# Performance work log

Hardware: AMD Instinct MI355X
Metric: run time of the kernel (lower is better)

The kernel has to match this reference:

```python
import jax, jax.numpy as jnp
import numpy as np
import math

MODEL_DIM = 1024
HEAD_DIM = 64
NUM_HEADS = 16
FF_MULT = 4
FF_DIM = FF_MULT * MODEL_DIM
ATTN_DIM = NUM_HEADS * HEAD_DIM
FUSED_DIMS = (ATTN_DIM, ATTN_DIM, ATTN_DIM, FF_DIM, FF_DIM)


def setup_inputs() -> dict:
    key = jax.random.key(0)
    k_x, k_in, k_attn, k_ff = jax.random.split(key, 4)
    B, S = 2, 2048
    inputs = jax.random.normal(k_x, (B, S, MODEL_DIM), dtype=jnp.float32)
    # LayerNorm affine params (torch defaults: weight=1, bias=0)
    ln_w = jnp.ones((MODEL_DIM,), dtype=jnp.float32)
    ln_b = jnp.zeros((MODEL_DIM,), dtype=jnp.float32)
    # Linear weights stored as [in, out] (equivalent to torch W.T)
    s_in = 1.0 / math.sqrt(MODEL_DIM)
    w_in = jax.random.uniform(k_in, (MODEL_DIM, sum(FUSED_DIMS)), jnp.float32, -s_in, s_in)
    s_a = 1.0 / math.sqrt(ATTN_DIM)
    w_attn = jax.random.uniform(k_attn, (ATTN_DIM, MODEL_DIM), jnp.float32, -s_a, s_a)
    s_f = 1.0 / math.sqrt(FF_DIM)
    w_ff = jax.random.uniform(k_ff, (FF_DIM, MODEL_DIM), jnp.float32, -s_f, s_f)
    return {"inputs": inputs, "ln_w": ln_w, "ln_b": ln_b,
            "w_in": w_in, "w_attn": w_attn, "w_ff": w_ff}


def _layer_norm(x, w, b, eps=1e-5):
    mu = jnp.mean(x, axis=-1, keepdims=True)
    var = jnp.var(x, axis=-1, keepdims=True)
    return (x - mu) * jax.lax.rsqrt(var + eps) * w + b


def reference(inputs, ln_w, ln_b, w_in, w_attn, w_ff):
    B, S, D = inputs.shape
    units = _layer_norm(inputs, ln_w, ln_b)
    proj = units @ w_in                                   # [B,S,3*A+2*F]
    splits = np.cumsum(FUSED_DIMS)[:-1]
    q, k, v, ff, ff_gate = jnp.split(proj, splits, axis=-1)
    # split heads: [B,S,H*d] -> [B,H,S,d]
    def heads(t):
        return t.reshape(B, S, NUM_HEADS, HEAD_DIM).transpose(0, 2, 1, 3)
    q, k, v = heads(q), heads(k), heads(v)
    scale = 1.0 / math.sqrt(HEAD_DIM)
    score = jnp.einsum('bhsd,bhTd->bhsT', q, k) * scale   # [B,H,S,S]
    weight = jax.nn.softmax(score, axis=-1)
    attn = jnp.einsum('bhsT,bhTd->bhsd', weight, v)       # [B,H,S,d]
    concat = attn.transpose(0, 2, 1, 3).reshape(B, S, ATTN_DIM)
    attn_out = concat @ w_attn                            # [B,S,D]
    ff_out = (ff * jax.nn.gelu(ff_gate, approximate=True)) @ w_ff
    return inputs + attn_out + ff_out
```

## Files before the change

### kernel.cpp

```cpp
#include <hip/hip_runtime.h>
#include <hip/hip_bf16.h>
#include <cstdint>
#include <cstddef>

typedef __bf16 bf16;
typedef __bf16 bf16x8 __attribute__((ext_vector_type(8)));
typedef float f32x4 __attribute__((ext_vector_type(4)));

#define MFMA16(a, b, c) __builtin_amdgcn_mfma_f32_16x16x32_bf16(a, b, c, 0, 0, 0)

#define GLOBAL_LOAD_LDS16(gptr, lptr)                                          \
  __builtin_amdgcn_global_load_lds(                                            \
      (const __attribute__((address_space(1))) void*)(gptr),                   \
      (__attribute__((address_space(3))) void*)(lptr), 16, 0, 0)

__global__ __launch_bounds__(256) void prep(const float* __restrict__ w_in,
                                            const float* __restrict__ w_attn,
                                            const float* __restrict__ w_ff,
                                            bf16* __restrict__ wt_in,
                                            bf16* __restrict__ wtcat,
                                            const float* __restrict__ x,
                                            const float* __restrict__ ln_w,
                                            const float* __restrict__ ln_b,
                                            bf16* __restrict__ xn) {
  __shared__ __align__(16) float t[64][65];
  const int tid = threadIdx.x;
  if (blockIdx.x < 4096) {
    int id = blockIdx.x;
    const float* src; bf16* dst;
    int srcN, n0, k0, kcol0;
    size_t LDO;
    bool win;
    if (id < 2816) {
      src = w_in; dst = wt_in; srcN = 11264; LDO = 1024;
      n0 = (id % 176) * 64; k0 = (id / 176) * 64; kcol0 = 0; win = true;
    } else if (id < 3072) {
      id -= 2816; src = w_attn; dst = wtcat; srcN = 1024; LDO = 5120;
      n0 = (id % 16) * 64; k0 = (id / 16) * 64; kcol0 = 0; win = false;
    } else {
      id -= 3072; src = w_ff; dst = wtcat; srcN = 1024; LDO = 5120;
      n0 = (id % 16) * 64; k0 = (id / 16) * 64; kcol0 = 1024; win = false;
    }
    int drow0;
    if (!win || n0 < 3072) {
      drow0 = n0;
    } else if (n0 < 7168) {
      int m = n0 - 3072; drow0 = 3072 + ((m >> 6) << 7);
    } else {
      int m = n0 - 7168; drow0 = 3072 + ((m >> 6) << 7) + 64;
    }
#pragma unroll
    for (int i = 0; i < 16; i++) {
      int k = i * 4 + (tid >> 6), n = tid & 63;
      t[k][n] = src[(size_t)(k0 + k) * srcN + n0 + n];
    }
    __syncthreads();
#pragma unroll
    for (int j = 0; j < 2; j++) {
      int n = j * 32 + (tid >> 3), kc = (tid & 7) * 8;
      bf16x8 o;
#pragma unroll
      for (int u = 0; u < 8; u++) o[u] = (bf16)t[kc + u][n];
      *(bf16x8*)&dst[(size_t)(drow0 + n) * LDO + kcol0 + k0 + kc] = o;
    }
  } else {
    __shared__ float rs[256], rss[256];
    const int row = blockIdx.x - 4096;
    const float* xr = x + (size_t)row * 1024;
    float4 v = *(const float4*)&xr[tid * 4];
    float s = v.x + v.y + v.z + v.w;
    float ss = v.x * v.x + v.y * v.y + v.z * v.z + v.w * v.w;
    rs[tid] = s; rss[tid] = ss;
    __syncthreads();
    for (int off = 128; off > 0; off >>= 1) {
      if (tid < off) { rs[tid] += rs[tid + off]; rss[tid] += rss[tid + off]; }
      __syncthreads();
    }
    const float mean = rs[0] * (1.f / 1024.f);
    const float var = rss[0] * (1.f / 1024.f) - mean * mean;
    const float rstd = rsqrtf(var + 1e-5f);
    const float* vp = (const float*)&v;
    for (int i = 0; i < 4; i++) {
      int c = tid * 4 + i;
      xn[(size_t)row * 1024 + c] = (bf16)((vp[i] - mean) * rstd * ln_w[c] + ln_b[c]);
    }
  }
}

__global__ __launch_bounds__(512, 4) void flash_attn(const bf16* __restrict__ proj,
                                                     const bf16* __restrict__ vt,
                                                     bf16* __restrict__ hcat) {
  __shared__ __align__(16) char smem[67584];
  bf16* Ks = (bf16*)smem;
  bf16* Vs = (bf16*)(smem + 16384);
  bf16* Ps = (bf16*)(smem + 32768);
  const int tid = threadIdx.x;
  const int wave = tid >> 6, lane = tid & 63;
  const int quad = lane >> 4, l16 = lane & 15;
  const int q0 = blockIdx.x * 128;
  const int h = blockIdx.y, b = blockIdx.z;
  constexpr size_t LDP = 3072;
  const bf16* Qb = proj + (size_t)b * 2048 * LDP + h * 64;
  const bf16* Kb = proj + (size_t)b * 2048 * LDP + 1024 + h * 64;
  const bf16* Vt = vt + (size_t)(b * 16 + h) * 64 * 2048;

  const int qrow = q0 + wave * 16 + l16;
  bf16x8 aq0r = *(const bf16x8*)&Qb[(size_t)qrow * LDP + quad * 8];
  bf16x8 aq1r = *(const bf16x8*)&Qb[(size_t)qrow * LDP + 32 + quad * 8];
  bf16x8 aq0, aq1;
#pragma unroll
  for (int i = 0; i < 8; i++) {
    aq0[i] = (bf16)((float)aq0r[i] * 0.125f);
    aq1[i] = (bf16)((float)aq1r[i] * 0.125f);
  }

  f32x4 O[4] = {};
  float plrow[4] = {0.f, 0.f, 0.f, 0.f};

  const int krow_ = wave * 8 + (lane >> 3);
  const int kq_ = ((lane & 7) ^ (krow_ & 7)) * 8;
  const int vrow_ = wave * 4 + (lane >> 4);
  const int vq_ = ((lane & 15) ^ (vrow_ & 15)) * 8;

  for (int j0 = 0; j0 < 2048; j0 += 128) {
#pragma unroll
    for (int p = 0; p < 2; p++) {
      int kr = p * 64 + krow_;
      GLOBAL_LOAD_LDS16(&Kb[(size_t)(j0 + kr) * LDP + kq_],
                        &Ks[kr * 64 + (lane & 7) * 8]);
      int vr = p * 32 + vrow_;
      GLOBAL_LOAD_LDS16(&Vt[(size_t)vr * 2048 + j0 + vq_],
                        &Vs[vr * 128 + (lane & 15) * 8]);
    }
    __syncthreads();

    f32x4 sa[8];
#pragma unroll
    for (int nt = 0; nt < 8; nt++) {
      int r = nt * 16 + l16;
      bf16x8 bk0 = *(const bf16x8*)&Ks[r * 64 + (quad ^ (r & 7)) * 8];
      bf16x8 bk1 = *(const bf16x8*)&Ks[r * 64 + ((quad + 4) ^ (r & 7)) * 8];
      f32x4 t = {};
      t = MFMA16(aq0, bk0, t);
      sa[nt] = MFMA16(aq1, bk1, t);
    }

    bf16* Pw = Ps + wave * (16 * 136);
#pragma unroll
    for (int r = 0; r < 4; r++) {
      bf16* pr = &Pw[(quad * 4 + r) * 136];
      float ts = 0.f;
#pragma unroll
      for (int nt = 0; nt < 8; nt++) {
        float p = __expf(sa[nt][r]);
        pr[nt * 16 + l16] = (bf16)p;
        ts += p;
      }
      plrow[r] += ts;
    }

#pragma unroll
    for (int kg = 0; kg < 4; kg++) {
      bf16x8 aP = *(const bf16x8*)&Pw[l16 * 136 + kg * 32 + quad * 8];
#pragma unroll
      for (int nb = 0; nb < 4; nb++) {
        int vrr = nb * 16 + l16;
        int vsl = ((kg * 4 + quad) ^ (vrr & 15)) * 8;
        bf16x8 bv = *(const bf16x8*)&Vs[vrr * 128 + vsl];
        O[nb] = MFMA16(aP, bv, O[nb]);
      }
    }
    __syncthreads();
  }

#pragma unroll
  for (int r = 0; r < 4; r++) {
    float ts = plrow[r];
#pragma unroll
    for (int d = 1; d < 16; d <<= 1) ts += __shfl_xor(ts, d, 64);
    float inv = 1.f / ts;
    size_t row = (size_t)b * 2048 + q0 + wave * 16 + quad * 4 + r;
#pragma unroll
    for (int nb = 0; nb < 4; nb++)
      hcat[row * 5120 + h * 64 + nb * 16 + l16] = (bf16)(O[nb][r] * inv);
  }
}

__global__ __launch_bounds__(512, 2) void gemm_proj(const bf16* __restrict__ A,
                                                    const bf16* __restrict__ Bt,
                                                    bf16* __restrict__ proj,
                                                    bf16* __restrict__ hcat,
                                                    bf16* __restrict__ vt) {
  constexpr int K = 1024, NT = 32;
  __shared__ __align__(16) char smem[98304];
  const int tid = threadIdx.x;
  const int wave = tid >> 6, lane = tid & 63;
  const int quad = lane >> 4, l16 = lane & 15;
  const int wm0 = (wave >> 2) * 128, wn0 = (wave & 3) * 64;

  const int id = (int)blockIdx.y * 44 + (int)blockIdx.x;
  const int xcd = id & 7, s = id >> 3;
  const int tx = (xcd & 3) * 11 + s % 11;
  const int ty = (xcd >> 2) * 8 + s / 11;

  const size_t rowA0 = (size_t)ty * 256;
  const size_t rowB0 = (size_t)tx * 256;
  const bf16* Ag = A + rowA0 * K;
  const bf16* Bg = Bt + rowB0 * K;

  const int srow = tid >> 2;
  const int sslot = tid & 3;
  const int rslot = (quad ^ ((l16 >> 1) & 3)) * 8;

  f32x4 acc[8][4] = {};

  auto STAGE = [&](int kt, int buf) {
    bf16* As = (bf16*)(smem + buf * 32768);
    bf16* Bs = As + 256 * 32;
    const int k0 = kt * 32;
#pragma unroll
    for (int p = 0; p < 2; p++) {
      int r = p * 128 + srow;
      int kq = (sslot ^ ((r >> 1) & 3)) * 8;
      GLOBAL_LOAD_LDS16(&Ag[(size_t)r * K + k0 + kq], &As[r * 32 + sslot * 8]);
      GLOBAL_LOAD_LDS16(&Bg[(size_t)r * K + k0 + kq], &Bs[r * 32 + sslot * 8]);
    }
  };

  STAGE(0, 0);
  STAGE(1, 1);
  asm volatile("s_waitcnt vmcnt(4)" ::: "memory");
  __builtin_amdgcn_s_barrier();
  asm volatile("" ::: "memory");

  int cbuf = 0, sbuf = 2;
#pragma unroll 1
  for (int kt = 0; kt < NT; kt++) {
    if (kt + 2 < NT) STAGE(kt + 2, sbuf);
    const bf16* As = (const bf16*)(smem + cbuf * 32768);
    const bf16* Bs = As + 256 * 32;
    bf16x8 bfr[4];
#pragma unroll
    for (int j = 0; j < 4; j++)
      bfr[j] = *(const bf16x8*)&Bs[(wn0 + j * 16 + l16) * 32 + rslot];
#pragma unroll
    for (int ih = 0; ih < 2; ih++) {
      bf16x8 af[4];
#pragma unroll
      for (int i = 0; i < 4; i++)
        af[i] = *(const bf16x8*)&As[(wm0 + (ih * 4 + i) * 16 + l16) * 32 + rslot];
      __builtin_amdgcn_s_setprio(1);
#pragma unroll
      for (int i = 0; i < 4; i++)
#pragma unroll
        for (int j = 0; j < 4; j++)
          acc[ih * 4 + i][j] = MFMA16(af[i], bfr[j], acc[ih * 4 + i][j]);
      __builtin_amdgcn_s_setprio(0);
    }
    if (kt + 2 < NT) {
      asm volatile("s_waitcnt vmcnt(4)" ::: "memory");
    } else {
      asm volatile("s_waitcnt vmcnt(0)" ::: "memory");
    }
    __builtin_amdgcn_s_barrier();
    asm volatile("" ::: "memory");
    cbuf = (cbuf == 2) ? 0 : cbuf + 1;
    sbuf = (sbuf == 2) ? 0 : sbuf + 1;
  }

  {
    const int xb = tx;
    const int T2 = xb - 12;
    bf16* Cs = (bf16*)smem;
    constexpr int LDC2 = 264;
#pragma unroll 1
    for (int h = 0; h < 2; h++) {
      if ((wave >> 2) == h) {
#pragma unroll
        for (int i = 0; i < 8; i++)
#pragma unroll
          for (int j = 0; j < 4; j++)
#pragma unroll
            for (int r = 0; r < 4; r++)
              Cs[(i * 16 + quad * 4 + r) * LDC2 + wn0 + j * 16 + l16] =
                  (bf16)acc[i][j][r];
      }
      __syncthreads();
      if (xb < 8) {
#pragma unroll
        for (int it = 0; it < 8; it++) {
          int idx = it * 512 + tid;
          int row = idx >> 5, ch = (idx & 31) * 8;
          *(bf16x8*)&proj[(rowA0 + h * 128 + row) * 3072 + rowB0 + ch] =
              *(const bf16x8*)&Cs[row * LDC2 + ch];
        }
      } else if (T2 < 0) {
        const int g0 = (int)rowA0 + h * 128;
        const int bb = g0 >> 11, sloc0 = g0 & 2047;
        const int hb = (xb - 8) * 4;
        bf16* vtb = vt + ((size_t)(bb * 16 + hb) * 64) * 2048 + sloc0;
#pragma unroll
        for (int it = 0; it < 8; it++) {
          int u = it * 512 + tid;
          int col = u & 255, sc = u >> 8;
          bf16x8 o;
#pragma unroll
          for (int k = 0; k < 8; k++) o[k] = Cs[(sc * 8 + k) * LDC2 + col];
          *(bf16x8*)&vtb[(size_t)col * 2048 + sc * 8] = o;
        }
      } else {
#pragma unroll
        for (int it = 0; it < 4; it++) {
          int idx = it * 512 + tid;
          int row = idx >> 4;
          int p = (idx >> 3) & 1, c8 = (idx & 7) * 8;
          bf16x8 f = *(const bf16x8*)&Cs[row * LDC2 + p * 128 + c8];
          bf16x8 g = *(const bf16x8*)&Cs[row * LDC2 + p * 128 + 64 + c8];
          bf16x8 o;
#pragma unroll
          for (int i = 0; i < 8; i++) {
            float xg = (float)g[i];
            float u = 0.7978845608f * (xg + 0.044715f * xg * xg * xg);
            float gl = xg / (1.f + __expf(-2.f * u));
            o[i] = (bf16)((float)f[i] * gl);
          }
          *(bf16x8*)&hcat[(rowA0 + h * 128 + row) * 5120 + 1024 +
                          (2 * T2 + p) * 64 + c8] = o;
        }
      }
      __syncthreads();
    }
  }
}

__global__ __launch_bounds__(512, 2) void gemm_out(const bf16* __restrict__ A,
                                                   const bf16* __restrict__ Bt,
                                                   bf16* __restrict__ part) {
  constexpr int LDAB = 5120, NT = 40;
  __shared__ __align__(16) char smem[98304];
  const int tid = threadIdx.x;
  const int wave = tid >> 6, lane = tid & 63;
  const int quad = lane >> 4, l16 = lane & 15;
  const int wm0 = (wave >> 2) * 128, wn0 = (wave & 3) * 64;

  const int id = (int)blockIdx.z * 64 + (int)blockIdx.y * 4 + (int)blockIdx.x;
  const int xcd = id & 7, s = id >> 3;
  const int tz = xcd >> 1;
  const int tx = s & 3;
  const int ty = (xcd & 1) * 8 + (s >> 2);

  const size_t rowA0 = (size_t)ty * 256;
  const size_t rowB0 = (size_t)tx * 256;
  const int kbeg = tz * 1280;
  const bf16* Ag = A + rowA0 * LDAB + kbeg;
  const bf16* Bg = Bt + rowB0 * LDAB + kbeg;

  const int srow = tid >> 2;
  const int sslot = tid & 3;
  const int rslot = (quad ^ ((l16 >> 1) & 3)) * 8;

  f32x4 acc[8][4] = {};

  auto STAGE = [&](int kt, int buf) {
    bf16* As = (bf16*)(smem + buf * 32768);
    bf16* Bs = As + 256 * 32;
    const int k0 = kt * 32;
#pragma unroll
    for (int p = 0; p < 2; p++) {
      int r = p * 128 + srow;
      int kq = (sslot ^ ((r >> 1) & 3)) * 8;
      GLOBAL_LOAD_LDS16(&Ag[(size_t)r * LDAB + k0 + kq], &As[r * 32 + sslot * 8]);
      GLOBAL_LOAD_LDS16(&Bg[(size_t)r * LDAB + k0 + kq], &Bs[r * 32 + sslot * 8]);
    }
  };

  STAGE(0, 0);
  STAGE(1, 1);
  asm volatile("s_waitcnt vmcnt(4)" ::: "memory");
  __builtin_amdgcn_s_barrier();
  asm volatile("" ::: "memory");

  int cbuf = 0, sbuf = 2;
#pragma unroll 1
  for (int kt = 0; kt < NT; kt++) {
    if (kt + 2 < NT) STAGE(kt + 2, sbuf);
    const bf16* As = (const bf16*)(smem + cbuf * 32768);
    const bf16* Bs = As + 256 * 32;
    bf16x8 bfr[4];
#pragma unroll
    for (int j = 0; j < 4; j++)
      bfr[j] = *(const bf16x8*)&Bs[(wn0 + j * 16 + l16) * 32 + rslot];
#pragma unroll
    for (int ih = 0; ih < 2; ih++) {
      bf16x8 af[4];
#pragma unroll
      for (int i = 0; i < 4; i++)
        af[i] = *(const bf16x8*)&As[(wm0 + (ih * 4 + i) * 16 + l16) * 32 + rslot];
      __builtin_amdgcn_s_setprio(1);
#pragma unroll
      for (int i = 0; i < 4; i++)
#pragma unroll
        for (int j = 0; j < 4; j++)
          acc[ih * 4 + i][j] = MFMA16(af[i], bfr[j], acc[ih * 4 + i][j]);
      __builtin_amdgcn_s_setprio(0);
    }
    if (kt + 2 < NT) {
      asm volatile("s_waitcnt vmcnt(4)" ::: "memory");
    } else {
      asm volatile("s_waitcnt vmcnt(0)" ::: "memory");
    }
    __builtin_amdgcn_s_barrier();
    asm volatile("" ::: "memory");
    cbuf = (cbuf == 2) ? 0 : cbuf + 1;
    sbuf = (sbuf == 2) ? 0 : sbuf + 1;
  }

  {
    bf16* dst = part + (size_t)tz * (4096 * 1024);
    bf16* Cs = (bf16*)smem;
    constexpr int LDC2 = 264;
#pragma unroll 1
    for (int h = 0; h < 2; h++) {
      if ((wave >> 2) == h) {
#pragma unroll
        for (int i = 0; i < 8; i++)
#pragma unroll
          for (int j = 0; j < 4; j++)
#pragma unroll
            for (int r = 0; r < 4; r++)
              Cs[(i * 16 + quad * 4 + r) * LDC2 + wn0 + j * 16 + l16] =
                  (bf16)acc[i][j][r];
      }
      __syncthreads();
#pragma unroll
      for (int it = 0; it < 8; it++) {
        int idx = it * 512 + tid;
        int row = idx >> 5, ch = (idx & 31) * 8;
        *(bf16x8*)&dst[(rowA0 + h * 128 + row) * 1024 + rowB0 + ch] =
            *(const bf16x8*)&Cs[row * LDC2 + ch];
      }
      __syncthreads();
    }
  }
}

__global__ __launch_bounds__(256) void reduce_out(const float* __restrict__ x,
                                                  const bf16* __restrict__ part,
                                                  float* __restrict__ out) {
  const size_t i = ((size_t)blockIdx.x * 256 + threadIdx.x) * 8;
  constexpr size_t SL = 4096 * 1024;
  float r[8];
  float4 x0 = *(const float4*)&x[i];
  float4 x1 = *(const float4*)&x[i + 4];
  r[0] = x0.x; r[1] = x0.y; r[2] = x0.z; r[3] = x0.w;
  r[4] = x1.x; r[5] = x1.y; r[6] = x1.z; r[7] = x1.w;
#pragma unroll
  for (int z = 0; z < 4; z++) {
    bf16x8 p = *(const bf16x8*)&part[z * SL + i];
#pragma unroll
    for (int k = 0; k < 8; k++) r[k] += (float)p[k];
  }
  float4 o0 = {r[0], r[1], r[2], r[3]};
  float4 o1 = {r[4], r[5], r[6], r[7]};
  *(float4*)&out[i] = o0;
  *(float4*)&out[i + 4] = o1;
}

extern "C" void kernel_launch(void* const* d_in, const int* in_sizes, int n_in,
                              void* d_out, int out_size, void* d_ws, size_t ws_size,
                              hipStream_t stream) {
  const float* x      = (const float*)d_in[0];
  const float* ln_w   = (const float*)d_in[1];
  const float* ln_b   = (const float*)d_in[2];
  const float* w_in   = (const float*)d_in[3];
  const float* w_attn = (const float*)d_in[4];
  const float* w_ff   = (const float*)d_in[5];
  float* out = (float*)d_out;
  char* ws = (char*)d_ws;

  bf16* wt_in = (bf16*)(ws);
  bf16* wtcat = (bf16*)(ws + 23068672);
  bf16* xn    = (bf16*)(ws + 33554432);
  bf16* proj  = (bf16*)(ws + 41943040);
  bf16* part  = (bf16*)(ws + 67108864);
  bf16* vt    = (bf16*)(ws + 100663296);
  bf16* hcat  = (bf16*)(ws + 134217728);

  prep<<<8192, 256, 0, stream>>>(w_in, w_attn, w_ff, wt_in, wtcat,
                                 x, ln_w, ln_b, xn);
  gemm_proj<<<dim3(44, 16), 512, 0, stream>>>(xn, wt_in, proj, hcat, vt);
  flash_attn<<<dim3(16, 16, 2), 512, 0, stream>>>(proj, vt, hcat);
  gemm_out<<<dim3(4, 16, 4), 512, 0, stream>>>(hcat, wtcat, part);
  reduce_out<<<2048, 256, 0, stream>>>(x, part, out);
}
```

Baseline: 354.0 us.

## Replace split-K partial buffers and reduce kernel with fp32 atomic accumulation

```diff
diff --git a/kernel.cpp b/kernel.cpp
--- a/kernel.cpp
+++ b/kernel.cpp
@@ -22,7 +22,8 @@
                                             const float* __restrict__ x,
                                             const float* __restrict__ ln_w,
                                             const float* __restrict__ ln_b,
-                                            bf16* __restrict__ xn) {
+                                            bf16* __restrict__ xn,
+                                            float* __restrict__ out) {
   __shared__ __align__(16) float t[64][65];
   const int tid = threadIdx.x;
   if (blockIdx.x < 4096) {
@@ -68,6 +69,7 @@
     const int row = blockIdx.x - 4096;
     const float* xr = x + (size_t)row * 1024;
     float4 v = *(const float4*)&xr[tid * 4];
+    *(float4*)&out[(size_t)row * 1024 + tid * 4] = v;
     float s = v.x + v.y + v.z + v.w;
     float ss = v.x * v.x + v.y * v.y + v.z * v.z + v.w * v.w;
     rs[tid] = s; rss[tid] = ss;
@@ -335,7 +337,7 @@
 
 __global__ __launch_bounds__(512, 2) void gemm_out(const bf16* __restrict__ A,
                                                    const bf16* __restrict__ Bt,
-                                                   bf16* __restrict__ part) {
+                                                   float* __restrict__ out) {
   constexpr int LDAB = 5120, NT = 40;
   __shared__ __align__(16) char smem[98304];
   const int tid = threadIdx.x;
@@ -415,55 +417,17 @@
     sbuf = (sbuf == 2) ? 0 : sbuf + 1;
   }
 
-  {
-    bf16* dst = part + (size_t)tz * (4096 * 1024);
-    bf16* Cs = (bf16*)smem;
-    constexpr int LDC2 = 264;
-#pragma unroll 1
-    for (int h = 0; h < 2; h++) {
-      if ((wave >> 2) == h) {
-#pragma unroll
-        for (int i = 0; i < 8; i++)
-#pragma unroll
-          for (int j = 0; j < 4; j++)
-#pragma unroll
-            for (int r = 0; r < 4; r++)
-              Cs[(i * 16 + quad * 4 + r) * LDC2 + wn0 + j * 16 + l16] =
-                  (bf16)acc[i][j][r];
-      }
-      __syncthreads();
-#pragma unroll
-      for (int it = 0; it < 8; it++) {
-        int idx = it * 512 + tid;
-        int row = idx >> 5, ch = (idx & 31) * 8;
-        *(bf16x8*)&dst[(rowA0 + h * 128 + row) * 1024 + rowB0 + ch] =
-            *(const bf16x8*)&Cs[row * LDC2 + ch];
-      }
-      __syncthreads();
-    }
-  }
-}
-
-__global__ __launch_bounds__(256) void reduce_out(const float* __restrict__ x,
-                                                  const bf16* __restrict__ part,
-                                                  float* __restrict__ out) {
-  const size_t i = ((size_t)blockIdx.x * 256 + threadIdx.x) * 8;
-  constexpr size_t SL = 4096 * 1024;
-  float r[8];
-  float4 x0 = *(const float4*)&x[i];
-  float4 x1 = *(const float4*)&x[i + 4];
-  r[0] = x0.x; r[1] = x0.y; r[2] = x0.z; r[3] = x0.w;
-  r[4] = x1.x; r[5] = x1.y; r[6] = x1.z; r[7] = x1.w;
-#pragma unroll
-  for (int z = 0; z < 4; z++) {
-    bf16x8 p = *(const bf16x8*)&part[z * SL + i];
-#pragma unroll
-    for (int k = 0; k < 8; k++) r[k] += (float)p[k];
-  }
-  float4 o0 = {r[0], r[1], r[2], r[3]};
-  float4 o1 = {r[4], r[5], r[6], r[7]};
-  *(float4*)&out[i] = o0;
-  *(float4*)&out[i + 4] = o1;
+#pragma unroll
+  for (int i = 0; i < 8; i++) {
+    size_t row = rowA0 + wm0 + i * 16 + quad * 4;
+#pragma unroll
+    for (int j = 0; j < 4; j++) {
+      size_t col = rowB0 + wn0 + j * 16 + l16;
+#pragma unroll
+      for (int r = 0; r < 4; r++)
+        atomicAdd(&out[(row + r) * 1024 + col], acc[i][j][r]);
+    }
+  }
 }
 
 extern "C" void kernel_launch(void* const* d_in, const int* in_sizes, int n_in,
@@ -482,14 +446,12 @@
   bf16* wtcat = (bf16*)(ws + 23068672);
   bf16* xn    = (bf16*)(ws + 33554432);
   bf16* proj  = (bf16*)(ws + 41943040);
-  bf16* part  = (bf16*)(ws + 67108864);
-  bf16* vt    = (bf16*)(ws + 100663296);
-  bf16* hcat  = (bf16*)(ws + 134217728);
+  bf16* vt    = (bf16*)(ws + 67108864);
+  bf16* hcat  = (bf16*)(ws + 75497472);
 
   prep<<<8192, 256, 0, stream>>>(w_in, w_attn, w_ff, wt_in, wtcat,
-                                 x, ln_w, ln_b, xn);
+                                 x, ln_w, ln_b, xn, out);
   gemm_proj<<<dim3(44, 16), 512, 0, stream>>>(xn, wt_in, proj, hcat, vt);
   flash_attn<<<dim3(16, 16, 2), 512, 0, stream>>>(proj, vt, hcat);
-  gemm_out<<<dim3(4, 16, 4), 512, 0, stream>>>(hcat, wtcat, part);
-  reduce_out<<<2048, 256, 0, stream>>>(x, part, out);
+  gemm_out<<<dim3(4, 16, 4), 512, 0, stream>>>(hcat, wtcat, out);
 }
```

Result: slower. 370.9 us (+4.8%).
